# Kernel optimization log

Hardware: AMD Instinct MI355X
Metric: run time of the kernel (lower is better)

The kernel has to match this reference:

```python
import jax, jax.numpy as jnp
import numpy as np

RCUT = 6.0
EPS = 1e-6
NUM_BASIS = 8
P = 6  # PolynomialSmooth envelope power
N_NODES = 100000
N_EDGES = 3200000
N_GRAPHS = 16

# 27 periodic image shifts: all integer combos of [-1,0,1]^3
_PERIODIC = jnp.asarray(
    np.stack(np.meshgrid(*([[-1, 0, 1]] * 3), indexing='ij'), -1).reshape(27, 3).astype(np.float32)
)


def _sh_lmax2(u):
    """e3nn spherical harmonics, lmax=2, normalize=True, normalization='component'.
    u: [E,3] unit vectors -> [E,9]."""
    x, y, z = u[..., 0], u[..., 1], u[..., 2]
    s3 = jnp.sqrt(jnp.asarray(3.0, u.dtype))
    s5 = jnp.sqrt(jnp.asarray(5.0, u.dtype))
    s15 = jnp.sqrt(jnp.asarray(15.0, u.dtype))
    return jnp.stack([
        jnp.ones_like(x),                      # l=0
        s3 * x, s3 * y, s3 * z,                # l=1
        s15 * x * z,                           # l=2
        s15 * x * y,
        s5 * (y * y - 0.5 * (x * x + z * z)),
        s15 * y * z,
        0.5 * s15 * (z * z - x * x),
    ], axis=-1)


def _bessel(lengths):
    # lengths: [E,1] -> [E,NUM_BASIS]
    k = jnp.arange(1, NUM_BASIS + 1, dtype=lengths.dtype) * jnp.pi / RCUT
    safe = jnp.clip(lengths, EPS, RCUT)
    return jnp.sin(safe * k) / (2.0 * safe)


def _poly_smooth(lengths):
    # standard polynomial envelope (DimeNet-style), zero at r=rcut
    x = jnp.clip(lengths / RCUT, 0.0, 1.0)
    c1 = (P + 1) * (P + 2) / 2.0
    c2 = float(P * (P + 2))
    c3 = P * (P + 1) / 2.0
    xp = x ** P
    return 1.0 - c1 * xp + c2 * xp * x - c3 * xp * x * x


def setup_inputs() -> dict:
    key = jax.random.key(0)
    k1, k2, k3, k4, k5 = jax.random.split(key, 5)
    pos = jax.random.normal(k1, (N_NODES, 3), dtype=jnp.float32) * 5.0
    cells = jax.random.normal(k2, (N_GRAPHS, 3, 3), dtype=jnp.float32)
    edge_index = jax.random.randint(k3, (2, N_EDGES), 0, N_NODES)
    periodic_index = jax.random.randint(k4, (N_EDGES,), 0, 27)
    batch = jnp.sort(jax.random.randint(k5, (N_NODES,), 0, N_GRAPHS))
    return {"pos": pos, "cells": cells, "edge_index": edge_index,
            "periodic_index": periodic_index, "batch": batch}


def reference(pos, cells, edge_index, periodic_index, batch):
    node_src, node_dst = edge_index[0], edge_index[1]
    vectors = pos[node_dst] - pos[node_src]                     # [E,3]
    shifts = _PERIODIC[periodic_index]                          # [E,3]
    src_cells = cells[batch[node_src]]                          # [E,3,3]
    vectors = vectors - jnp.einsum('eij,ei->ej', src_cells, shifts)
    vectors = -vectors                                          # dst == 'atom'
    lengths = jnp.linalg.norm(vectors, axis=-1, keepdims=True)  # [E,1]
    unit = vectors / jnp.maximum(lengths, EPS)                  # normalize=True
    attr = _sh_lmax2(unit)                                      # [E,9]
    basis = _bessel(lengths)                                    # [E,8]
    cutoff = _poly_smooth(lengths)                              # [E,1]
    basis_weight = basis * cutoff                               # [E,8]
    # pack (length, sh attr, smooth, basis_weight) -> [E,19]
    return jnp.concatenate([lengths, attr, cutoff, basis_weight], axis=-1)
```

## Files before the change

kernel.cpp:

```cpp
#include <hip/hip_runtime.h>

#define BLOCK 256

__global__ __launch_bounds__(BLOCK) void edge_encoding_kernel(
    const float* __restrict__ pos,
    const float* __restrict__ cells,
    const int*  __restrict__ eidx,
    const int*  __restrict__ pidx,
    const int*  __restrict__ batch,
    float* __restrict__ out,
    int E)
{
    __shared__ float s_cells[144];
    __shared__ __align__(16) float s_out[BLOCK * 19];

    const int tid = threadIdx.x;
    if (tid < 144) s_cells[tid] = cells[tid];
    __syncthreads();

    const int base = blockIdx.x * BLOCK;
    const int e = base + tid;

    float row[19];
    if (e < E) {
        const int src = eidx[e];
        const int dst = eidx[E + e];
        const int p   = pidx[e];
        const int g   = batch[src];

        const float sx = pos[3*src+0], sy = pos[3*src+1], sz = pos[3*src+2];
        const float dx = pos[3*dst+0], dy = pos[3*dst+1], dz = pos[3*dst+2];

        const float f0 = (float)(p / 9 - 1);
        const float f1 = (float)((p / 3) % 3 - 1);
        const float f2 = (float)(p % 3 - 1);

        const float* C = s_cells + g * 9;
        const float tx = C[0]*f0 + C[3]*f1 + C[6]*f2;
        const float ty = C[1]*f0 + C[4]*f1 + C[7]*f2;
        const float tz = C[2]*f0 + C[5]*f1 + C[8]*f2;

        const float vx = sx - dx + tx;
        const float vy = sy - dy + ty;
        const float vz = sz - dz + tz;

        const float len  = sqrtf(vx*vx + vy*vy + vz*vz);
        const float invl = 1.0f / fmaxf(len, 1e-6f);
        const float x = vx * invl, y = vy * invl, z = vz * invl;

        const float s3  = 1.7320508075688772f;
        const float s5  = 2.2360679774997896f;
        const float s15 = 3.872983346207417f;

        row[0] = len;
        row[1] = 1.0f;
        row[2] = s3 * x;
        row[3] = s3 * y;
        row[4] = s3 * z;
        row[5] = s15 * x * z;
        row[6] = s15 * x * y;
        row[7] = s5  * (y*y - 0.5f*(x*x + z*z));
        row[8] = s15 * y * z;
        row[9] = 0.5f * s15 * (z*z - x*x);

        const float xc = fminf(len * (1.0f/6.0f), 1.0f);
        const float x3 = xc * xc * xc;
        const float x6 = x3 * x3;
        const float cut = fmaf(x6, fmaf(xc, fmaf(-21.0f, xc, 48.0f), -28.0f), 1.0f);
        row[10] = cut;

        const float safe = fminf(fmaxf(len, 1e-6f), 6.0f);
        const float a = safe * 0.5235987755982988f;
        float sa, ca;
        sincosf(a, &sa, &ca);
        const float w = cut / (2.0f * safe);
        const float two_ca = 2.0f * ca;
        float s_prev = 0.0f, s_cur = sa;
        row[11] = s_cur * w;
        #pragma unroll
        for (int n = 2; n <= 8; ++n) {
            const float s_next = two_ca * s_cur - s_prev;
            s_prev = s_cur;
            s_cur  = s_next;
            row[10 + n] = s_cur * w;
        }
    } else {
        #pragma unroll
        for (int j = 0; j < 19; ++j) row[j] = 0.0f;
    }

    #pragma unroll
    for (int j = 0; j < 19; ++j) s_out[tid * 19 + j] = row[j];
    __syncthreads();

    const int nvalid  = min(BLOCK, E - base);
    const int nfloats = nvalid * 19;
    float* gout = out + (size_t)base * 19;
    const int n4 = nfloats >> 2;
    const float4* s4 = reinterpret_cast<const float4*>(s_out);
    float4* g4 = reinterpret_cast<float4*>(gout);
    for (int i = tid; i < n4; i += BLOCK) g4[i] = s4[i];
    for (int i = (n4 << 2) + tid; i < nfloats; i += BLOCK) gout[i] = s_out[i];
}

extern "C" void kernel_launch(void* const* d_in, const int* in_sizes, int n_in,
                              void* d_out, int out_size, void* d_ws, size_t ws_size,
                              hipStream_t stream) {
    const float* pos   = (const float*)d_in[0];
    const float* cells = (const float*)d_in[1];
    const int*   eidx  = (const int*)d_in[2];
    const int*   pidx  = (const int*)d_in[3];
    const int*   batch = (const int*)d_in[4];
    float* out = (float*)d_out;

    const int E = in_sizes[3];
    const int grid = (E + BLOCK - 1) / BLOCK;
    edge_encoding_kernel<<<grid, BLOCK, 0, stream>>>(pos, cells, eidx, pidx, batch, out, E);
}
```

Baseline: 313.4 us.

## Pack node positions with batch id into float4 and use nontemporal loads/stores

```diff
diff --git a/kernel.cpp b/kernel.cpp
--- a/kernel.cpp
+++ b/kernel.cpp
@@ -2,12 +2,33 @@
 
 #define BLOCK 256
 
-__global__ __launch_bounds__(BLOCK) void edge_encoding_kernel(
+typedef float vf4 __attribute__((ext_vector_type(4)));
+
+extern "C" __global__ void __launch_bounds__(BLOCK) pack_pos_batch(
     const float* __restrict__ pos,
+    const int*  __restrict__ batch,
+    vf4* __restrict__ pos4,
+    int N)
+{
+    const int i = blockIdx.x * BLOCK + threadIdx.x;
+    if (i < N) {
+        vf4 v;
+        v.x = pos[3 * i + 0];
+        v.y = pos[3 * i + 1];
+        v.z = pos[3 * i + 2];
+        v.w = __int_as_float(batch[i]);
+        pos4[i] = v;
+    }
+}
+
+template <bool PACKED>
+__global__ void __launch_bounds__(BLOCK) edge_encoding_kernel(
+    const float* __restrict__ pos,
+    const vf4*   __restrict__ pos4,
     const float* __restrict__ cells,
-    const int*  __restrict__ eidx,
-    const int*  __restrict__ pidx,
-    const int*  __restrict__ batch,
+    const int*   __restrict__ eidx,
+    const int*   __restrict__ pidx,
+    const int*   __restrict__ batch,
     float* __restrict__ out,
     int E)
 {
@@ -23,13 +44,23 @@
 
     float row[19];
     if (e < E) {
-        const int src = eidx[e];
-        const int dst = eidx[E + e];
-        const int p   = pidx[e];
-        const int g   = batch[src];
+        const int src = __builtin_nontemporal_load(eidx + e);
+        const int dst = __builtin_nontemporal_load(eidx + E + e);
+        const int p   = __builtin_nontemporal_load(pidx + e);
 
-        const float sx = pos[3*src+0], sy = pos[3*src+1], sz = pos[3*src+2];
-        const float dx = pos[3*dst+0], dy = pos[3*dst+1], dz = pos[3*dst+2];
+        float sx, sy, sz, dx, dy, dz;
+        int g;
+        if (PACKED) {
+            const vf4 ps = pos4[src];
+            const vf4 pd = pos4[dst];
+            sx = ps.x; sy = ps.y; sz = ps.z;
+            dx = pd.x; dy = pd.y; dz = pd.z;
+            g  = __float_as_int(ps.w);
+        } else {
+            sx = pos[3*src+0]; sy = pos[3*src+1]; sz = pos[3*src+2];
+            dx = pos[3*dst+0]; dy = pos[3*dst+1]; dz = pos[3*dst+2];
+            g  = batch[src];
+        }
 
         const float f0 = (float)(p / 9 - 1);
         const float f1 = (float)((p / 3) % 3 - 1);
@@ -71,8 +102,8 @@
 
         const float safe = fminf(fmaxf(len, 1e-6f), 6.0f);
         const float a = safe * 0.5235987755982988f;
-        float sa, ca;
-        sincosf(a, &sa, &ca);
+        const float sa = __sinf(a);
+        const float ca = __cosf(a);
         const float w = cut / (2.0f * safe);
         const float two_ca = 2.0f * ca;
         float s_prev = 0.0f, s_cur = sa;
@@ -97,10 +128,12 @@
     const int nfloats = nvalid * 19;
     float* gout = out + (size_t)base * 19;
     const int n4 = nfloats >> 2;
-    const float4* s4 = reinterpret_cast<const float4*>(s_out);
-    float4* g4 = reinterpret_cast<float4*>(gout);
-    for (int i = tid; i < n4; i += BLOCK) g4[i] = s4[i];
-    for (int i = (n4 << 2) + tid; i < nfloats; i += BLOCK) gout[i] = s_out[i];
+    const vf4* s4 = reinterpret_cast<const vf4*>(s_out);
+    vf4* g4 = reinterpret_cast<vf4*>(gout);
+    for (int i = tid; i < n4; i += BLOCK)
+        __builtin_nontemporal_store(s4[i], g4 + i);
+    for (int i = (n4 << 2) + tid; i < nfloats; i += BLOCK)
+        __builtin_nontemporal_store(s_out[i], gout + i);
 }
 
 extern "C" void kernel_launch(void* const* d_in, const int* in_sizes, int n_in,
@@ -114,6 +147,17 @@
     float* out = (float*)d_out;
 
     const int E = in_sizes[3];
+    const int N = in_sizes[4];
     const int grid = (E + BLOCK - 1) / BLOCK;
-    edge_encoding_kernel<<<grid, BLOCK, 0, stream>>>(pos, cells, eidx, pidx, batch, out, E);
+
+    if (d_ws != nullptr && ws_size >= (size_t)N * sizeof(vf4)) {
+        vf4* pos4 = (vf4*)d_ws;
+        const int pgrid = (N + BLOCK - 1) / BLOCK;
+        pack_pos_batch<<<pgrid, BLOCK, 0, stream>>>(pos, batch, pos4, N);
+        edge_encoding_kernel<true><<<grid, BLOCK, 0, stream>>>(
+            pos, pos4, cells, eidx, pidx, batch, out, E);
+    } else {
+        edge_encoding_kernel<false><<<grid, BLOCK, 0, stream>>>(
+            pos, nullptr, cells, eidx, pidx, batch, out, E);
+    }
 }
```

Result: faster. 294.6 us (median of 2 runs) (-6.0%).
